# Kernel optimization log

Measured on AMD Instinct MI355X. Metric: run time of the kernel, lower is better.

## Reference

```python
import jax, jax.numpy as jnp
import numpy as np

EPS = 1e-05  # config.norm_eps
C = 4        # len('qkvm')

def setup_inputs() -> dict:
    key = jax.random.key(0)
    k1, k2, k3 = jax.random.split(key, 3)
    B, T, D = 4, 4096, 4096
    L_TOT = 48  # (lidx+2)*C with lidx=10
    x = jax.random.normal(k1, (B, T, D), dtype=jnp.float32)
    # torch Linear weights are [out_features, in_features]
    W1 = jax.random.normal(k2, (L_TOT, D), dtype=jnp.float32) * (D ** -0.5)
    W2 = jax.random.normal(k3, (L_TOT, L_TOT), dtype=jnp.float32) * (L_TOT ** -0.5)
    return {"x": x, "W1": W1, "W2": W2}

def reference(x, W1, W2):
    # RMSNorm without scale
    var = jnp.mean(x * x, axis=-1, keepdims=True)
    xn = x * jax.lax.rsqrt(var + EPS)                      # [B, T, D]
    h = jnp.einsum('btd,ld->btl', xn, W1)                  # [B, T, l]
    dw = jnp.einsum('btk,lk->btl', jax.nn.gelu(h, approximate=False), W2)
    B, T, Ltot = dw.shape
    # rearrange 'B T (C L) -> C B T L'
    return jnp.transpose(dw.reshape(B, T, C, Ltot // C), (2, 0, 1, 3))
```

## Files before the change

kernel.cpp:

```cpp
#include <hip/hip_runtime.h>
#include <hip/hip_bf16.h>

#define DDIM 4096
#define LTOT 48
#define BQ 4
#define TT 4096

typedef __attribute__((ext_vector_type(4))) float f32x4;
typedef __attribute__((ext_vector_type(8))) short bf16x8;

__device__ __forceinline__ void gload_lds16(const void* g, void* l) {
    __builtin_amdgcn_global_load_lds(
        (const __attribute__((address_space(1))) void*)g,
        (__attribute__((address_space(3))) void*)l, 16, 0, 0);
}

__device__ __forceinline__ unsigned cvt_pk(float x, float y) {
    union { __hip_bfloat162 h; unsigned u; } c;
    c.h = __float22bfloat162_rn(make_float2(x, y));
    return c.u;
}

__global__ void w1cvt_kernel(const float* __restrict__ w1, ushort* __restrict__ w1b) {
    int i = blockIdx.x * 256 + threadIdx.x;
    union { float f; unsigned u; } v; v.f = w1[i];
    unsigned r = v.u + 0x7fffu + ((v.u >> 16) & 1u);
    w1b[i] = (ushort)(r >> 16);
}

__global__ __launch_bounds__(256, 4) void fused_kernel(
        const float* __restrict__ x,
        const ushort* __restrict__ w1b,
        const float* __restrict__ w2,
        float* __restrict__ out) {
    __shared__ __align__(1024) char smem[32768];
    __shared__ float ssw[4][16];
    __shared__ float scl[16];

    const int tid  = threadIdx.x;
    const int wave = tid >> 6;
    const int lane = tid & 63;
    const int rl   = lane & 15;
    const int kg   = lane >> 4;
    const int row0 = blockIdx.x * 16;
    const int kw   = wave * 1024;

    char* wbase = smem + wave * 8192;

    int dso[2][2];
    #pragma unroll
    for (int h = 0; h < 2; ++h)
        #pragma unroll
        for (int p = 0; p < 2; ++p)
            dso[h][p] = rl * 256 + (((h * 8 + kg * 2 + p) ^ rl) << 4);

    auto stage = [&](int t) {
        const int kb = kw + t * 64;
        char* lb = wbase + (t & 1) * 4096;
        #pragma unroll
        for (int i = 0; i < 4; ++i) {
            int rloc = i * 4 + kg;
            int blkg = rl ^ rloc;
            const float* src = x + (size_t)(row0 + rloc) * DDIM + kb + blkg * 4;
            gload_lds16(src, lb + i * 1024);
        }
    };

    auto loadB = [&](int s, bf16x8 (&bl)[6]) {
        const ushort* bp = w1b + (size_t)rl * DDIM + kw + s * 64 + kg * 8;
        #pragma unroll
        for (int n = 0; n < 3; ++n)
            #pragma unroll
            for (int h = 0; h < 2; ++h)
                bl[n * 2 + h] = *(const bf16x8*)(bp + n * 16 * DDIM + h * 32);
    };

    float ss = 0.f;
    f32x4 acc[3] = {{0.f,0.f,0.f,0.f},{0.f,0.f,0.f,0.f},{0.f,0.f,0.f,0.f}};
    bf16x8 bA[6], bB[6];

    stage(0); stage(1); loadB(0, bA);

    auto body = [&](int s, bf16x8 (&bu)[6], bf16x8 (&bl)[6]) {
        asm volatile("s_waitcnt vmcnt(4)" ::: "memory");
        char* lb = wbase + (s & 1) * 4096;
        f32x4 a[2][2];
        #pragma unroll
        for (int h = 0; h < 2; ++h)
            #pragma unroll
            for (int p = 0; p < 2; ++p)
                a[h][p] = *(const f32x4*)(lb + dso[h][p]);
        if (s < 15) loadB(s + 1, bl);
        #pragma unroll
        for (int h = 0; h < 2; ++h) {
            f32x4 a0 = a[h][0], a1 = a[h][1];
            ss = fmaf(a0.x, a0.x, ss); ss = fmaf(a0.y, a0.y, ss);
            ss = fmaf(a0.z, a0.z, ss); ss = fmaf(a0.w, a0.w, ss);
            ss = fmaf(a1.x, a1.x, ss); ss = fmaf(a1.y, a1.y, ss);
            ss = fmaf(a1.z, a1.z, ss); ss = fmaf(a1.w, a1.w, ss);
            union { bf16x8 v; unsigned u[4]; } af;
            af.u[0] = cvt_pk(a0.x, a0.y); af.u[1] = cvt_pk(a0.z, a0.w);
            af.u[2] = cvt_pk(a1.x, a1.y); af.u[3] = cvt_pk(a1.z, a1.w);
            #pragma unroll
            for (int n = 0; n < 3; ++n)
                acc[n] = __builtin_amdgcn_mfma_f32_16x16x32_bf16(
                             af.v, bu[n * 2 + h], acc[n], 0, 0, 0);
        }
        asm volatile("s_waitcnt lgkmcnt(0)" ::: "memory");
        if (s < 14) stage(s + 2);
    };

    for (int sp = 0; sp < 8; ++sp) {
        body(2 * sp,     bA, bB);
        body(2 * sp + 1, bB, bA);
    }

    ss += __shfl_xor(ss, 16);
    ss += __shfl_xor(ss, 32);
    if (lane < 16) ssw[wave][lane] = ss;
    __syncthreads();

    float* dots = (float*)smem;
    float* gbuf = (float*)(smem + 12288);
    float* w2s  = (float*)(smem + 15360);

    #pragma unroll
    for (int n = 0; n < 3; ++n)
        #pragma unroll
        for (int i = 0; i < 4; ++i)
            dots[(wave * 16 + kg * 4 + i) * 48 + n * 16 + rl] = acc[n][i];
    for (int i = tid; i < LTOT * LTOT; i += 256) w2s[i] = w2[i];
    __syncthreads();

    if (tid < 16) {
        float st = ssw[0][tid] + ssw[1][tid] + ssw[2][tid] + ssw[3][tid];
        scl[tid] = rsqrtf(st * (1.0f / (float)DDIM) + 1e-5f);
    }
    __syncthreads();

    #pragma unroll
    for (int i = 0; i < 3; ++i) {
        int v = tid + i * 256;
        int row = v / 48, col = v - row * 48;
        float d = dots[(0 * 16 + row) * 48 + col] + dots[(1 * 16 + row) * 48 + col]
                + dots[(2 * 16 + row) * 48 + col] + dots[(3 * 16 + row) * 48 + col];
        float h = d * scl[row];
        gbuf[row * 48 + col] = h * 0.5f * (1.0f + erff(h * 0.70710678118654752f));
    }
    __syncthreads();

    #pragma unroll
    for (int i = 0; i < 3; ++i) {
        int v = tid + i * 256;
        int row = v / 48, l = v - row * 48;
        float sacc = 0.f;
        #pragma unroll
        for (int k = 0; k < LTOT; ++k)
            sacc = fmaf(gbuf[row * 48 + k], w2s[l * LTOT + k], sacc);
        int rg = row0 + row;
        int b  = rg >> 12;
        int t  = rg & 4095;
        int c  = l / 12, j = l - c * 12;
        out[(((size_t)(c * BQ + b) * TT + t) * 12) + j] = sacc;
    }
}

extern "C" void kernel_launch(void* const* d_in, const int* in_sizes, int n_in,
                              void* d_out, int out_size, void* d_ws, size_t ws_size,
                              hipStream_t stream) {
    const float* x  = (const float*)d_in[0];
    const float* W1 = (const float*)d_in[1];
    const float* W2 = (const float*)d_in[2];
    float* out = (float*)d_out;
    ushort* w1b = (ushort*)d_ws;

    w1cvt_kernel<<<(LTOT * DDIM) / 256, 256, 0, stream>>>(W1, w1b);
    fused_kernel<<<(BQ * TT) / 16, 256, 0, stream>>>(x, w1b, W2, out);
}
```

Baseline: 70.90 us.

## Use single-wave blocks covering full K per 16-row tile, dropping cross-wave reductions

Each block becomes one 64-lane wave that walks the whole 4096-wide K dimension for 16 rows. The x tile is staged in 16 KB chunks with double-buffered global-to-LDS loads, and W1 fragments are double-buffered in registers. This removes the four-way K split, the cross-wave LDS reduction of dots and sums of squares, and the block barriers. The epilogue is vectorised with f32x4 loads of W2 and f32x4 output stores. In exchange each block has only one wave with 32 KB of LDS and a longer serial loop, so latency hiding depends on occupancy across blocks.

```diff
diff --git a/kernel.cpp b/kernel.cpp
--- a/kernel.cpp
+++ b/kernel.cpp
@@ -3,8 +3,6 @@
 
 #define DDIM 4096
 #define LTOT 48
-#define BQ 4
-#define TT 4096
 
 typedef __attribute__((ext_vector_type(4))) float f32x4;
 typedef __attribute__((ext_vector_type(8))) short bf16x8;
@@ -28,141 +26,148 @@
     w1b[i] = (ushort)(r >> 16);
 }
 
-__global__ __launch_bounds__(256, 4) void fused_kernel(
+__global__ __launch_bounds__(64, 1) void fused_kernel(
         const float* __restrict__ x,
         const ushort* __restrict__ w1b,
         const float* __restrict__ w2,
         float* __restrict__ out) {
     __shared__ __align__(1024) char smem[32768];
-    __shared__ float ssw[4][16];
-    __shared__ float scl[16];
 
-    const int tid  = threadIdx.x;
-    const int wave = tid >> 6;
-    const int lane = tid & 63;
+    const int lane = threadIdx.x;
     const int rl   = lane & 15;
     const int kg   = lane >> 4;
     const int row0 = blockIdx.x * 16;
-    const int kw   = wave * 1024;
 
-    char* wbase = smem + wave * 8192;
-
-    int dso[2][2];
-    #pragma unroll
-    for (int h = 0; h < 2; ++h)
+    auto stage = [&](int c) {
+        char* lb = smem + (c & 1) * 16384;
+        const float* xb = x + (size_t)row0 * DDIM + c * 256;
         #pragma unroll
-        for (int p = 0; p < 2; ++p)
-            dso[h][p] = rl * 256 + (((h * 8 + kg * 2 + p) ^ rl) << 4);
-
-    auto stage = [&](int t) {
-        const int kb = kw + t * 64;
-        char* lb = wbase + (t & 1) * 4096;
-        #pragma unroll
-        for (int i = 0; i < 4; ++i) {
-            int rloc = i * 4 + kg;
-            int blkg = rl ^ rloc;
-            const float* src = x + (size_t)(row0 + rloc) * DDIM + kb + blkg * 4;
-            gload_lds16(src, lb + i * 1024);
+        for (int r = 0; r < 16; ++r) {
+            int sblk = (lane & 48) | ((lane ^ r) & 15);
+            gload_lds16(xb + (size_t)r * DDIM + sblk * 4, lb + r * 1024);
         }
     };
 
-    auto loadB = [&](int s, bf16x8 (&bl)[6]) {
-        const ushort* bp = w1b + (size_t)rl * DDIM + kw + s * 64 + kg * 8;
+    auto loadB = [&](int s, bf16x8 (&bf)[6]) {
+        const ushort* bp = w1b + (size_t)rl * DDIM + s * 64 + kg * 8;
         #pragma unroll
         for (int n = 0; n < 3; ++n)
             #pragma unroll
             for (int h = 0; h < 2; ++h)
-                bl[n * 2 + h] = *(const bf16x8*)(bp + n * 16 * DDIM + h * 32);
+                bf[n * 2 + h] = *(const bf16x8*)(bp + n * 16 * DDIM + h * 32);
     };
 
+    bf16x8 breg[2][6];
+    f32x4 acc[3] = {{0.f,0.f,0.f,0.f},{0.f,0.f,0.f,0.f},{0.f,0.f,0.f,0.f}};
     float ss = 0.f;
-    f32x4 acc[3] = {{0.f,0.f,0.f,0.f},{0.f,0.f,0.f,0.f},{0.f,0.f,0.f,0.f}};
-    bf16x8 bA[6], bB[6];
 
-    stage(0); stage(1); loadB(0, bA);
+    loadB(0, breg[0]);
+    stage(0);
 
-    auto body = [&](int s, bf16x8 (&bu)[6], bf16x8 (&bl)[6]) {
-        asm volatile("s_waitcnt vmcnt(4)" ::: "memory");
-        char* lb = wbase + (s & 1) * 4096;
-        f32x4 a[2][2];
+    #pragma unroll
+    for (int c = 0; c < 16; ++c) {
+        if (c == 0) asm volatile("s_waitcnt vmcnt(0)" ::: "memory");
+        else        asm volatile("s_waitcnt vmcnt(24)" ::: "memory");
+
+        const char* lb = smem + (c & 1) * 16384;
+        f32x4 a[4][2][2];
         #pragma unroll
-        for (int h = 0; h < 2; ++h)
+        for (int t = 0; t < 4; ++t)
             #pragma unroll
-            for (int p = 0; p < 2; ++p)
-                a[h][p] = *(const f32x4*)(lb + dso[h][p]);
-        if (s < 15) loadB(s + 1, bl);
+            for (int h = 0; h < 2; ++h)
+                #pragma unroll
+                for (int p = 0; p < 2; ++p) {
+                    int g   = t * 16 + h * 8 + kg * 2 + p;
+                    int pos = (g & 48) | ((g ^ rl) & 15);
+                    a[t][h][p] = *(const f32x4*)(lb + rl * 1024 + pos * 16);
+                }
+        asm volatile("s_waitcnt lgkmcnt(0)" ::: "memory");
+        __builtin_amdgcn_sched_barrier(0);
+        if (c < 15) stage(c + 1);
+        __builtin_amdgcn_sched_barrier(0);
+        asm volatile("" ::: "memory");
+
         #pragma unroll
-        for (int h = 0; h < 2; ++h) {
-            f32x4 a0 = a[h][0], a1 = a[h][1];
-            ss = fmaf(a0.x, a0.x, ss); ss = fmaf(a0.y, a0.y, ss);
-            ss = fmaf(a0.z, a0.z, ss); ss = fmaf(a0.w, a0.w, ss);
-            ss = fmaf(a1.x, a1.x, ss); ss = fmaf(a1.y, a1.y, ss);
-            ss = fmaf(a1.z, a1.z, ss); ss = fmaf(a1.w, a1.w, ss);
-            union { bf16x8 v; unsigned u[4]; } af;
-            af.u[0] = cvt_pk(a0.x, a0.y); af.u[1] = cvt_pk(a0.z, a0.w);
-            af.u[2] = cvt_pk(a1.x, a1.y); af.u[3] = cvt_pk(a1.z, a1.w);
+        for (int t = 0; t < 4; ++t) {
+            const int s = c * 4 + t;
+            if (s + 1 < 64) loadB(s + 1, breg[(s + 1) & 1]);
             #pragma unroll
-            for (int n = 0; n < 3; ++n)
-                acc[n] = __builtin_amdgcn_mfma_f32_16x16x32_bf16(
-                             af.v, bu[n * 2 + h], acc[n], 0, 0, 0);
+            for (int h = 0; h < 2; ++h) {
+                f32x4 a0 = a[t][h][0], a1 = a[t][h][1];
+                ss = fmaf(a0.x, a0.x, ss); ss = fmaf(a0.y, a0.y, ss);
+                ss = fmaf(a0.z, a0.z, ss); ss = fmaf(a0.w, a0.w, ss);
+                ss = fmaf(a1.x, a1.x, ss); ss = fmaf(a1.y, a1.y, ss);
+                ss = fmaf(a1.z, a1.z, ss); ss = fmaf(a1.w, a1.w, ss);
+                union { bf16x8 v; unsigned u[4]; } af;
+                af.u[0] = cvt_pk(a0.x, a0.y); af.u[1] = cvt_pk(a0.z, a0.w);
+                af.u[2] = cvt_pk(a1.x, a1.y); af.u[3] = cvt_pk(a1.z, a1.w);
+                #pragma unroll
+                for (int n = 0; n < 3; ++n)
+                    acc[n] = __builtin_amdgcn_mfma_f32_16x16x32_bf16(
+                                 af.v, breg[s & 1][n * 2 + h], acc[n], 0, 0, 0);
+            }
         }
-        asm volatile("s_waitcnt lgkmcnt(0)" ::: "memory");
-        if (s < 14) stage(s + 2);
-    };
+    }
 
-    for (int sp = 0; sp < 8; ++sp) {
-        body(2 * sp,     bA, bB);
-        body(2 * sp + 1, bB, bA);
-    }
+    asm volatile("s_waitcnt vmcnt(0) lgkmcnt(0)" ::: "memory");
 
     ss += __shfl_xor(ss, 16);
     ss += __shfl_xor(ss, 32);
-    if (lane < 16) ssw[wave][lane] = ss;
-    __syncthreads();
+    const float scl = rsqrtf(ss * (1.0f / (float)DDIM) + 1e-5f);
 
     float* dots = (float*)smem;
-    float* gbuf = (float*)(smem + 12288);
-    float* w2s  = (float*)(smem + 15360);
+    float* gbuf = (float*)(smem + 3072);
+    float* w2s  = (float*)(smem + 6144);
 
     #pragma unroll
     for (int n = 0; n < 3; ++n)
         #pragma unroll
         for (int i = 0; i < 4; ++i)
-            dots[(wave * 16 + kg * 4 + i) * 48 + n * 16 + rl] = acc[n][i];
-    for (int i = tid; i < LTOT * LTOT; i += 256) w2s[i] = w2[i];
-    __syncthreads();
-
-    if (tid < 16) {
-        float st = ssw[0][tid] + ssw[1][tid] + ssw[2][tid] + ssw[3][tid];
-        scl[tid] = rsqrtf(st * (1.0f / (float)DDIM) + 1e-5f);
-    }
-    __syncthreads();
+            dots[(kg * 4 + i) * 48 + n * 16 + rl] = acc[n][i];
 
     #pragma unroll
-    for (int i = 0; i < 3; ++i) {
-        int v = tid + i * 256;
-        int row = v / 48, col = v - row * 48;
-        float d = dots[(0 * 16 + row) * 48 + col] + dots[(1 * 16 + row) * 48 + col]
-                + dots[(2 * 16 + row) * 48 + col] + dots[(3 * 16 + row) * 48 + col];
-        float h = d * scl[row];
-        gbuf[row * 48 + col] = h * 0.5f * (1.0f + erff(h * 0.70710678118654752f));
+    for (int i = 0; i < 9; ++i) {
+        int v = lane + i * 64;
+        f32x4 w = *(const f32x4*)(w2 + v * 4);
+        *(f32x4*)(w2s + v * 4) = w;
     }
-    __syncthreads();
+    asm volatile("s_waitcnt lgkmcnt(0)" ::: "memory");
 
     #pragma unroll
-    for (int i = 0; i < 3; ++i) {
-        int v = tid + i * 256;
-        int row = v / 48, l = v - row * 48;
+    for (int j = 0; j < 12; ++j) {
+        float h = dots[rl * 48 + kg * 12 + j] * scl;
+        gbuf[rl * 48 + kg * 12 + j] = h * 0.5f * (1.0f + erff(h * 0.70710678118654752f));
+    }
+    asm volatile("s_waitcnt lgkmcnt(0)" ::: "memory");
+
+    f32x4 grow[12];
+    #pragma unroll
+    for (int q = 0; q < 12; ++q)
+        grow[q] = *(const f32x4*)(gbuf + rl * 48 + q * 4);
+
+    float o[12];
+    #pragma unroll
+    for (int jj = 0; jj < 12; ++jj) {
+        const int l = kg * 12 + jj;
         float sacc = 0.f;
         #pragma unroll
-        for (int k = 0; k < LTOT; ++k)
-            sacc = fmaf(gbuf[row * 48 + k], w2s[l * LTOT + k], sacc);
-        int rg = row0 + row;
-        int b  = rg >> 12;
-        int t  = rg & 4095;
-        int c  = l / 12, j = l - c * 12;
-        out[(((size_t)(c * BQ + b) * TT + t) * 12) + j] = sacc;
+        for (int q = 0; q < 12; ++q) {
+            f32x4 wv = *(const f32x4*)(w2s + l * 48 + q * 4);
+            sacc = fmaf(grow[q].x, wv.x, sacc);
+            sacc = fmaf(grow[q].y, wv.y, sacc);
+            sacc = fmaf(grow[q].z, wv.z, sacc);
+            sacc = fmaf(grow[q].w, wv.w, sacc);
+        }
+        o[jj] = sacc;
     }
+
+    const int rg = row0 + rl;
+    const int b  = rg >> 12;
+    const int t  = rg & 4095;
+    float* op = out + ((size_t)(kg * 4 + b) * 4096 + t) * 12;
+    *(f32x4*)(op + 0) = {o[0], o[1], o[2],  o[3]};
+    *(f32x4*)(op + 4) = {o[4], o[5], o[6],  o[7]};
+    *(f32x4*)(op + 8) = {o[8], o[9], o[10], o[11]};
 }
 
 extern "C" void kernel_launch(void* const* d_in, const int* in_sizes, int n_in,
@@ -175,5 +180,5 @@
     ushort* w1b = (ushort*)d_ws;
 
     w1cvt_kernel<<<(LTOT * DDIM) / 256, 256, 0, stream>>>(W1, w1b);
-    fused_kernel<<<(BQ * TT) / 16, 256, 0, stream>>>(x, w1b, W2, out);
+    fused_kernel<<<16384 / 16, 64, 0, stream>>>(x, w1b, W2, out);
 }
```

Result: slower. 72.63 us (+2.5%).

## Load x directly to registers instead of staging through LDS

Applied to the files above, without the earlier changes.

Replaces the global_load_lds staging of x into swizzled shared memory with direct per-lane vector loads into registers, double-buffered together with the W1 fragments. This removes the LDS round trip, the explicit waitcnt handling and the swizzle addressing, and shrinks shared memory so more blocks can fit per CU. In exchange the register pressure rises, and each lane's 16-byte loads now stride across rows, which may coalesce less well than the LDS-staged pattern.

```diff
diff --git a/kernel.cpp b/kernel.cpp
--- a/kernel.cpp
+++ b/kernel.cpp
@@ -3,17 +3,9 @@
 
 #define DDIM 4096
 #define LTOT 48
-#define BQ 4
-#define TT 4096
 
 typedef __attribute__((ext_vector_type(4))) float f32x4;
 typedef __attribute__((ext_vector_type(8))) short bf16x8;
-
-__device__ __forceinline__ void gload_lds16(const void* g, void* l) {
-    __builtin_amdgcn_global_load_lds(
-        (const __attribute__((address_space(1))) void*)g,
-        (__attribute__((address_space(3))) void*)l, 16, 0, 0);
-}
 
 __device__ __forceinline__ unsigned cvt_pk(float x, float y) {
     union { __hip_bfloat162 h; unsigned u; } c;
@@ -33,9 +25,11 @@
         const ushort* __restrict__ w1b,
         const float* __restrict__ w2,
         float* __restrict__ out) {
-    __shared__ __align__(1024) char smem[32768];
+    __shared__ float dots[4][16][48];
     __shared__ float ssw[4][16];
     __shared__ float scl[16];
+    __shared__ float gbuf[16][48];
+    __shared__ float w2s[LTOT * LTOT];
 
     const int tid  = threadIdx.x;
     const int wave = tid >> 6;
@@ -45,55 +39,33 @@
     const int row0 = blockIdx.x * 16;
     const int kw   = wave * 1024;
 
-    char* wbase = smem + wave * 8192;
+    const float*  xp = x   + (size_t)(row0 + rl) * DDIM + kw + kg * 8;
+    const ushort* bp = w1b + (size_t)rl * DDIM          + kw + kg * 8;
 
-    int dso[2][2];
-    #pragma unroll
-    for (int h = 0; h < 2; ++h)
+    auto loadA = [&](int c, f32x4 (&A)[2][2]) {
+        const float* p = xp + c * 64;
         #pragma unroll
-        for (int p = 0; p < 2; ++p)
-            dso[h][p] = rl * 256 + (((h * 8 + kg * 2 + p) ^ rl) << 4);
-
-    auto stage = [&](int t) {
-        const int kb = kw + t * 64;
-        char* lb = wbase + (t & 1) * 4096;
-        #pragma unroll
-        for (int i = 0; i < 4; ++i) {
-            int rloc = i * 4 + kg;
-            int blkg = rl ^ rloc;
-            const float* src = x + (size_t)(row0 + rloc) * DDIM + kb + blkg * 4;
-            gload_lds16(src, lb + i * 1024);
+        for (int h = 0; h < 2; ++h) {
+            A[h][0] = *(const f32x4*)(p + h * 32);
+            A[h][1] = *(const f32x4*)(p + h * 32 + 4);
         }
     };
-
-    auto loadB = [&](int s, bf16x8 (&bl)[6]) {
-        const ushort* bp = w1b + (size_t)rl * DDIM + kw + s * 64 + kg * 8;
+    auto loadB = [&](int c, bf16x8 (&Bv)[6]) {
+        const ushort* p = bp + c * 64;
         #pragma unroll
         for (int n = 0; n < 3; ++n)
             #pragma unroll
             for (int h = 0; h < 2; ++h)
-                bl[n * 2 + h] = *(const bf16x8*)(bp + n * 16 * DDIM + h * 32);
+                Bv[n * 2 + h] = *(const bf16x8*)(p + n * 16 * DDIM + h * 32);
     };
 
+    f32x4 acc[3] = {{0.f,0.f,0.f,0.f},{0.f,0.f,0.f,0.f},{0.f,0.f,0.f,0.f}};
     float ss = 0.f;
-    f32x4 acc[3] = {{0.f,0.f,0.f,0.f},{0.f,0.f,0.f,0.f},{0.f,0.f,0.f,0.f}};
-    bf16x8 bA[6], bB[6];
 
-    stage(0); stage(1); loadB(0, bA);
-
-    auto body = [&](int s, bf16x8 (&bu)[6], bf16x8 (&bl)[6]) {
-        asm volatile("s_waitcnt vmcnt(4)" ::: "memory");
-        char* lb = wbase + (s & 1) * 4096;
-        f32x4 a[2][2];
-        #pragma unroll
-        for (int h = 0; h < 2; ++h)
-            #pragma unroll
-            for (int p = 0; p < 2; ++p)
-                a[h][p] = *(const f32x4*)(lb + dso[h][p]);
-        if (s < 15) loadB(s + 1, bl);
+    auto compute = [&](f32x4 (&A)[2][2], bf16x8 (&Bv)[6]) {
         #pragma unroll
         for (int h = 0; h < 2; ++h) {
-            f32x4 a0 = a[h][0], a1 = a[h][1];
+            f32x4 a0 = A[h][0], a1 = A[h][1];
             ss = fmaf(a0.x, a0.x, ss); ss = fmaf(a0.y, a0.y, ss);
             ss = fmaf(a0.z, a0.z, ss); ss = fmaf(a0.w, a0.w, ss);
             ss = fmaf(a1.x, a1.x, ss); ss = fmaf(a1.y, a1.y, ss);
@@ -104,31 +76,33 @@
             #pragma unroll
             for (int n = 0; n < 3; ++n)
                 acc[n] = __builtin_amdgcn_mfma_f32_16x16x32_bf16(
-                             af.v, bu[n * 2 + h], acc[n], 0, 0, 0);
+                             af.v, Bv[n * 2 + h], acc[n], 0, 0, 0);
         }
-        asm volatile("s_waitcnt lgkmcnt(0)" ::: "memory");
-        if (s < 14) stage(s + 2);
     };
 
+    f32x4 A0[2][2], A1[2][2];
+    bf16x8 B0[6], B1[6];
+    loadA(0, A0); loadB(0, B0);
+    loadA(1, A1); loadB(1, B1);
+
     for (int sp = 0; sp < 8; ++sp) {
-        body(2 * sp,     bA, bB);
-        body(2 * sp + 1, bB, bA);
+        const int c = 2 * sp;
+        compute(A0, B0);
+        if (c + 2 < 16) { loadA(c + 2, A0); loadB(c + 2, B0); }
+        compute(A1, B1);
+        if (c + 3 < 16) { loadA(c + 3, A1); loadB(c + 3, B1); }
     }
 
     ss += __shfl_xor(ss, 16);
     ss += __shfl_xor(ss, 32);
     if (lane < 16) ssw[wave][lane] = ss;
-    __syncthreads();
-
-    float* dots = (float*)smem;
-    float* gbuf = (float*)(smem + 12288);
-    float* w2s  = (float*)(smem + 15360);
 
     #pragma unroll
     for (int n = 0; n < 3; ++n)
         #pragma unroll
         for (int i = 0; i < 4; ++i)
-            dots[(wave * 16 + kg * 4 + i) * 48 + n * 16 + rl] = acc[n][i];
+            dots[wave][kg * 4 + i][n * 16 + rl] = acc[n][i];
+
     for (int i = tid; i < LTOT * LTOT; i += 256) w2s[i] = w2[i];
     __syncthreads();
 
@@ -142,10 +116,10 @@
     for (int i = 0; i < 3; ++i) {
         int v = tid + i * 256;
         int row = v / 48, col = v - row * 48;
-        float d = dots[(0 * 16 + row) * 48 + col] + dots[(1 * 16 + row) * 48 + col]
-                + dots[(2 * 16 + row) * 48 + col] + dots[(3 * 16 + row) * 48 + col];
+        float d = dots[0][row][col] + dots[1][row][col]
+                + dots[2][row][col] + dots[3][row][col];
         float h = d * scl[row];
-        gbuf[row * 48 + col] = h * 0.5f * (1.0f + erff(h * 0.70710678118654752f));
+        gbuf[row][col] = h * 0.5f * (1.0f + erff(h * 0.70710678118654752f));
     }
     __syncthreads();
 
@@ -156,12 +130,12 @@
         float sacc = 0.f;
         #pragma unroll
         for (int k = 0; k < LTOT; ++k)
-            sacc = fmaf(gbuf[row * 48 + k], w2s[l * LTOT + k], sacc);
+            sacc = fmaf(gbuf[row][k], w2s[l * LTOT + k], sacc);
         int rg = row0 + row;
         int b  = rg >> 12;
         int t  = rg & 4095;
-        int c  = l / 12, j = l - c * 12;
-        out[(((size_t)(c * BQ + b) * TT + t) * 12) + j] = sacc;
+        int cc = l / 12, j = l - cc * 12;
+        out[(((size_t)(cc * 4 + b) * 4096 + t) * 12) + j] = sacc;
     }
 }
 
@@ -175,5 +149,5 @@
     ushort* w1b = (ushort*)d_ws;
 
     w1cvt_kernel<<<(LTOT * DDIM) / 256, 256, 0, stream>>>(W1, w1b);
-    fused_kernel<<<(BQ * TT) / 16, 256, 0, stream>>>(x, w1b, W2, out);
+    fused_kernel<<<16384 / 16, 256, 0, stream>>>(x, w1b, W2, out);
 }
```

After: 85.65 us. 1.21x slower.
